# Kernel tuning notes

Hardware: AMD Instinct MI355X
Metric: run time of the kernel (lower is better)

Reference implementation:

```python
import jax, jax.numpy as jnp
import numpy as np

B = 2097152  # flattened batch of 3x3 rotation matrices

def setup_inputs() -> dict:
    key = jax.random.key(0)
    k1, k2 = jax.random.split(key)
    # scale by 0.1 so cos=(trace(m1 m2^T)-1)/2 stays strictly inside (-1,1)
    pred_rot = jax.random.normal(k1, (B, 3, 3), dtype=jnp.float32) * 0.1
    gt_rot = jax.random.normal(k2, (B, 3, 3), dtype=jnp.float32) * 0.1
    return {"pred_rot": pred_rot, "gt_rot": gt_rot}

def reference(pred_rot, gt_rot):
    m1 = pred_rot.reshape(-1, 3, 3)
    m2 = gt_rot.reshape(-1, 3, 3)
    # trace(m1 @ m2^T) == sum(m1 * m2) elementwise -> avoid the bmm
    cos = (jnp.einsum('bij,bij->b', m1, m2) - 1.0) * 0.5
    cos = jnp.clip(cos, -1.0, 1.0)  # min with +1, max with -1
    theta = jnp.arccos(cos)
    return jnp.mean(theta)  # reduction='mean'
```

## Files before the change

### kernel.cpp

```cpp
#include <hip/hip_runtime.h>
#include <math.h>


#define TPB 256
#define MPT 4

__global__ __launch_bounds__(TPB, 2) void geo_kernel(
    const float* __restrict__ a, const float* __restrict__ b,
    float* __restrict__ out, float invM, int M)
{
    const long long t  = (long long)blockIdx.x * TPB + threadIdx.x;
    const long long m0 = t * (long long)MPT;
    float sum = 0.0f;

    if (m0 + MPT <= M) {
        const float4* __restrict__ a4 = (const float4*)a + t * 9;
        const float4* __restrict__ b4 = (const float4*)b + t * 9;
        float4 A0 = a4[0], A1 = a4[1], A2 = a4[2], A3 = a4[3], A4 = a4[4],
               A5 = a4[5], A6 = a4[6], A7 = a4[7], A8 = a4[8];
        float4 B0 = b4[0], B1 = b4[1], B2 = b4[2], B3 = b4[3], B4 = b4[4],
               B5 = b4[5], B6 = b4[6], B7 = b4[7], B8 = b4[8];

        float c0 = A0.x * B0.x;
        c0 = fmaf(A0.y, B0.y, c0); c0 = fmaf(A0.z, B0.z, c0);
        c0 = fmaf(A0.w, B0.w, c0); c0 = fmaf(A1.x, B1.x, c0);
        c0 = fmaf(A1.y, B1.y, c0); c0 = fmaf(A1.z, B1.z, c0);
        c0 = fmaf(A1.w, B1.w, c0); c0 = fmaf(A2.x, B2.x, c0);
        float c1 = A2.y * B2.y;
        c1 = fmaf(A2.z, B2.z, c1); c1 = fmaf(A2.w, B2.w, c1);
        c1 = fmaf(A3.x, B3.x, c1); c1 = fmaf(A3.y, B3.y, c1);
        c1 = fmaf(A3.z, B3.z, c1); c1 = fmaf(A3.w, B3.w, c1);
        c1 = fmaf(A4.x, B4.x, c1); c1 = fmaf(A4.y, B4.y, c1);
        float c2 = A4.z * B4.z;
        c2 = fmaf(A4.w, B4.w, c2); c2 = fmaf(A5.x, B5.x, c2);
        c2 = fmaf(A5.y, B5.y, c2); c2 = fmaf(A5.z, B5.z, c2);
        c2 = fmaf(A5.w, B5.w, c2); c2 = fmaf(A6.x, B6.x, c2);
        c2 = fmaf(A6.y, B6.y, c2); c2 = fmaf(A6.z, B6.z, c2);
        float c3 = A6.w * B6.w;
        c3 = fmaf(A7.x, B7.x, c3); c3 = fmaf(A7.y, B7.y, c3);
        c3 = fmaf(A7.z, B7.z, c3); c3 = fmaf(A7.w, B7.w, c3);
        c3 = fmaf(A8.x, B8.x, c3); c3 = fmaf(A8.y, B8.y, c3);
        c3 = fmaf(A8.z, B8.z, c3); c3 = fmaf(A8.w, B8.w, c3);

        c0 = fminf(1.0f, fmaxf(-1.0f, (c0 - 1.0f) * 0.5f));
        c1 = fminf(1.0f, fmaxf(-1.0f, (c1 - 1.0f) * 0.5f));
        c2 = fminf(1.0f, fmaxf(-1.0f, (c2 - 1.0f) * 0.5f));
        c3 = fminf(1.0f, fmaxf(-1.0f, (c3 - 1.0f) * 0.5f));
        sum = (acosf(c0) + acosf(c1)) + (acosf(c2) + acosf(c3));
    } else {
        for (int j = 0; j < MPT; ++j) {
            long long m = m0 + j;
            if (m < M) {
                float c = 0.0f;
                for (int k = 0; k < 9; ++k)
                    c = fmaf(a[m * 9 + k], b[m * 9 + k], c);
                float cosv = fminf(1.0f, fmaxf(-1.0f, (c - 1.0f) * 0.5f));
                sum += acosf(cosv);
            }
        }
    }

    #pragma unroll
    for (int off = 32; off > 0; off >>= 1)
        sum += __shfl_down(sum, off, 64);
    __shared__ float ws[TPB / 64];
    const int lane = threadIdx.x & 63;
    const int wid  = threadIdx.x >> 6;
    if (lane == 0) ws[wid] = sum;
    __syncthreads();
    if (threadIdx.x == 0) {
        float s = 0.0f;
        #pragma unroll
        for (int i = 0; i < TPB / 64; ++i) s += ws[i];
        atomicAdd(out, s * invM);
    }
}

extern "C" void kernel_launch(void* const* d_in, const int* in_sizes, int n_in,
                              void* d_out, int out_size, void* d_ws, size_t ws_size,
                              hipStream_t stream) {
    const float* a = (const float*)d_in[0];
    const float* b = (const float*)d_in[1];
    float* out = (float*)d_out;

    const int n = in_sizes[0];
    const int M = n / 9;

    const int nthreads = (M + MPT - 1) / MPT;
    const int grid     = (nthreads + TPB - 1) / TPB;

    hipMemsetAsync(out, 0, (size_t)out_size * sizeof(float), stream);
    geo_kernel<<<grid, TPB, 0, stream>>>(a, b, out, 1.0f / (float)M, M);
}
```

Measured before the change: 169.7 us.

## Stage tiles through LDS with direct global-to-LDS loads for coalescing

Replaces the per-thread strided float4 loads with coalesced global_load_lds transfers that copy a 512-matrix tile of each input straight into shared memory. Threads then read their 9-element rows from LDS, with each thread handling 2 matrices instead of 4. The aim is fully coalesced, contiguous global reads and fewer vector registers. The cost is a block-wide barrier before compute, about 36KB of LDS per block which limits occupancy, and possible LDS bank conflicts from the stride-9 reads.

```diff
diff --git a/kernel.cpp b/kernel.cpp
--- a/kernel.cpp
+++ b/kernel.cpp
@@ -3,59 +3,69 @@
 
 
 #define TPB 256
-#define MPT 4
+#define MPB 512
+#define FLOATS_PER_IN 4608
+#define F4_PER_IN 1152
 
-__global__ __launch_bounds__(TPB, 2) void geo_kernel(
+typedef const __attribute__((address_space(1))) float4 g_f4;
+typedef __attribute__((address_space(3))) float4 l_f4;
+
+__global__ __launch_bounds__(TPB) void geo_kernel(
     const float* __restrict__ a, const float* __restrict__ b,
     float* __restrict__ out, float invM, int M)
 {
-    const long long t  = (long long)blockIdx.x * TPB + threadIdx.x;
-    const long long m0 = t * (long long)MPT;
+    __shared__ float lds[2 * FLOATS_PER_IN];
+    __shared__ float wsum[TPB / 64];
+
+    const int tid = threadIdx.x;
+    const long long tile_m0 = (long long)blockIdx.x * MPB;
     float sum = 0.0f;
 
-    if (m0 + MPT <= M) {
-        const float4* __restrict__ a4 = (const float4*)a + t * 9;
-        const float4* __restrict__ b4 = (const float4*)b + t * 9;
-        float4 A0 = a4[0], A1 = a4[1], A2 = a4[2], A3 = a4[3], A4 = a4[4],
-               A5 = a4[5], A6 = a4[6], A7 = a4[7], A8 = a4[8];
-        float4 B0 = b4[0], B1 = b4[1], B2 = b4[2], B3 = b4[3], B4 = b4[4],
-               B5 = b4[5], B6 = b4[6], B7 = b4[7], B8 = b4[8];
+    if (tile_m0 + MPB <= M) {
+        const float4* a4 = (const float4*)(a + tile_m0 * 9);
+        const float4* b4 = (const float4*)(b + tile_m0 * 9);
+        const int wave_base = tid & ~63;
 
-        float c0 = A0.x * B0.x;
-        c0 = fmaf(A0.y, B0.y, c0); c0 = fmaf(A0.z, B0.z, c0);
-        c0 = fmaf(A0.w, B0.w, c0); c0 = fmaf(A1.x, B1.x, c0);
-        c0 = fmaf(A1.y, B1.y, c0); c0 = fmaf(A1.z, B1.z, c0);
-        c0 = fmaf(A1.w, B1.w, c0); c0 = fmaf(A2.x, B2.x, c0);
-        float c1 = A2.y * B2.y;
-        c1 = fmaf(A2.z, B2.z, c1); c1 = fmaf(A2.w, B2.w, c1);
-        c1 = fmaf(A3.x, B3.x, c1); c1 = fmaf(A3.y, B3.y, c1);
-        c1 = fmaf(A3.z, B3.z, c1); c1 = fmaf(A3.w, B3.w, c1);
-        c1 = fmaf(A4.x, B4.x, c1); c1 = fmaf(A4.y, B4.y, c1);
-        float c2 = A4.z * B4.z;
-        c2 = fmaf(A4.w, B4.w, c2); c2 = fmaf(A5.x, B5.x, c2);
-        c2 = fmaf(A5.y, B5.y, c2); c2 = fmaf(A5.z, B5.z, c2);
-        c2 = fmaf(A5.w, B5.w, c2); c2 = fmaf(A6.x, B6.x, c2);
-        c2 = fmaf(A6.y, B6.y, c2); c2 = fmaf(A6.z, B6.z, c2);
-        float c3 = A6.w * B6.w;
-        c3 = fmaf(A7.x, B7.x, c3); c3 = fmaf(A7.y, B7.y, c3);
-        c3 = fmaf(A7.z, B7.z, c3); c3 = fmaf(A7.w, B7.w, c3);
-        c3 = fmaf(A8.x, B8.x, c3); c3 = fmaf(A8.y, B8.y, c3);
-        c3 = fmaf(A8.z, B8.z, c3); c3 = fmaf(A8.w, B8.w, c3);
+        #pragma unroll
+        for (int k = 0; k < 4; ++k) {
+            const int idx = k * 256 + tid;
+            const int uni = k * 256 + wave_base;
+            __builtin_amdgcn_global_load_lds((g_f4*)(a4 + idx),
+                (l_f4*)((float4*)lds + uni), 16, 0, 0);
+            __builtin_amdgcn_global_load_lds((g_f4*)(b4 + idx),
+                (l_f4*)((float4*)lds + F4_PER_IN + uni), 16, 0, 0);
+        }
+        if (tid < 128) {
+            const int idx = 1024 + tid;
+            const int uni = 1024 + wave_base;
+            __builtin_amdgcn_global_load_lds((g_f4*)(a4 + idx),
+                (l_f4*)((float4*)lds + uni), 16, 0, 0);
+            __builtin_amdgcn_global_load_lds((g_f4*)(b4 + idx),
+                (l_f4*)((float4*)lds + F4_PER_IN + uni), 16, 0, 0);
+        }
+        __syncthreads();
 
-        c0 = fminf(1.0f, fmaxf(-1.0f, (c0 - 1.0f) * 0.5f));
-        c1 = fminf(1.0f, fmaxf(-1.0f, (c1 - 1.0f) * 0.5f));
-        c2 = fminf(1.0f, fmaxf(-1.0f, (c2 - 1.0f) * 0.5f));
-        c3 = fminf(1.0f, fmaxf(-1.0f, (c3 - 1.0f) * 0.5f));
-        sum = (acosf(c0) + acosf(c1)) + (acosf(c2) + acosf(c3));
+        const float* al = lds;
+        const float* bl = lds + FLOATS_PER_IN;
+        #pragma unroll
+        for (int c = 0; c < 2; ++c) {
+            float d = 0.0f;
+            #pragma unroll
+            for (int j = 0; j < 9; ++j)
+                d = fmaf(al[9 * tid + 2304 * c + j],
+                         bl[9 * tid + 2304 * c + j], d);
+            float cv = fminf(1.0f, fmaxf(-1.0f, (d - 1.0f) * 0.5f));
+            sum += acosf(cv);
+        }
     } else {
-        for (int j = 0; j < MPT; ++j) {
-            long long m = m0 + j;
+        for (int c = 0; c < 2; ++c) {
+            long long m = tile_m0 + tid + 256 * c;
             if (m < M) {
-                float c = 0.0f;
-                for (int k = 0; k < 9; ++k)
-                    c = fmaf(a[m * 9 + k], b[m * 9 + k], c);
-                float cosv = fminf(1.0f, fmaxf(-1.0f, (c - 1.0f) * 0.5f));
-                sum += acosf(cosv);
+                float d = 0.0f;
+                for (int j = 0; j < 9; ++j)
+                    d = fmaf(a[m * 9 + j], b[m * 9 + j], d);
+                float cv = fminf(1.0f, fmaxf(-1.0f, (d - 1.0f) * 0.5f));
+                sum += acosf(cv);
             }
         }
     }
@@ -63,15 +73,14 @@
     #pragma unroll
     for (int off = 32; off > 0; off >>= 1)
         sum += __shfl_down(sum, off, 64);
-    __shared__ float ws[TPB / 64];
-    const int lane = threadIdx.x & 63;
-    const int wid  = threadIdx.x >> 6;
-    if (lane == 0) ws[wid] = sum;
+    const int lane = tid & 63;
+    const int wid  = tid >> 6;
+    if (lane == 0) wsum[wid] = sum;
     __syncthreads();
-    if (threadIdx.x == 0) {
+    if (tid == 0) {
         float s = 0.0f;
         #pragma unroll
-        for (int i = 0; i < TPB / 64; ++i) s += ws[i];
+        for (int i = 0; i < TPB / 64; ++i) s += wsum[i];
         atomicAdd(out, s * invM);
     }
 }
@@ -86,8 +95,7 @@
     const int n = in_sizes[0];
     const int M = n / 9;
 
-    const int nthreads = (M + MPT - 1) / MPT;
-    const int grid     = (nthreads + TPB - 1) / TPB;
+    const int grid = (M + MPB - 1) / MPB;
 
     hipMemsetAsync(out, 0, (size_t)out_size * sizeof(float), stream);
     geo_kernel<<<grid, TPB, 0, stream>>>(a, b, out, 1.0f / (float)M, M);
```

Measured after the change: 178.2 us. 1.05x slower.
